# Performance work log

Hardware: AMD Instinct MI355X
Metric: run time of the kernel (lower is better)

Reference implementation:

```python
import jax, jax.numpy as jnp
import numpy as np

EPS = 1e-06


def setup_inputs() -> dict:
    key = jax.random.key(0)
    kq, kk, kv = jax.random.split(key, 3)
    B, H, T, P = 2, 8, 1024, 64
    Q = jax.random.normal(kq, (B, H, T, P), dtype=jnp.float32)
    K = jax.random.normal(kk, (B, H, T, P), dtype=jnp.float32)
    V = jax.random.normal(kv, (B, H, T, P), dtype=jnp.float32)
    return {"Q": Q, "K": K, "V": V}


def _scan_attention(Q, K, V):
    Q_feat = jnp.exp(Q)                                  # (B,H,T,P)
    K_feat = jnp.exp(K)                                  # (B,H,T,P)
    m0 = jnp.log(K_feat)                                 # (B,H,T,P)
    N0 = jnp.einsum('bhtp,bhtn->bhtpn', V, K_feat)       # (B,H,T,P,P) matrix state
    D0 = K_feat                                          # (B,H,T,P)

    def combine(x, y):
        m_x, N_x, D_x = x
        m_y, N_y, D_y = y
        m_new = jnp.maximum(m_x, m_y)
        scale_x = jnp.exp(m_x - m_new)
        scale_y = jnp.exp(m_y - m_new)
        N_new = N_x * scale_x[..., None] + N_y * scale_y[..., None]
        D_new = D_x * scale_x + D_y * scale_y
        return (m_new, N_new, D_new)

    m_cum, num_cum, denom_cum = jax.lax.associative_scan(combine, (m0, N0, D0), axis=2)

    Y_num = jnp.einsum('bhtp,bhtpq->bhtq', Q_feat, num_cum)   # (B,H,T,P)
    Y_den = jnp.einsum('bhtp,bhtp->bht', Q_feat, denom_cum)   # (B,H,T)
    Y = Y_num / (Y_den[..., None] + EPS)
    B, H, T, P = Q.shape
    return Y.transpose(0, 2, 1, 3).reshape(B, T, H * P)


def reference(Q, K, V):
    return _scan_attention(Q, K, V)
```

## Files before the change

### kernel.cpp

```cpp
#include <hip/hip_runtime.h>
#include <hip/hip_bf16.h>

#define TDIM 1024
#define PDIM 64
#define BHN  16
#define NCH  64
#define CHS  16

typedef __bf16 bf16_t;
typedef bf16_t bf16x8 __attribute__((ext_vector_type(8)));
typedef float  floatx4 __attribute__((ext_vector_type(4)));

__device__ __forceinline__ floatx4 mfma16(bf16x8 a, bf16x8 b, floatx4 c) {
    return __builtin_amdgcn_mfma_f32_16x16x32_bf16(a, b, c, 0, 0, 0);
}

__global__ __launch_bounds__(64) void stats_kernel(
        const float* __restrict__ K,
        float* __restrict__ cmax, float* __restrict__ csum) {
    int bh = blockIdx.x >> 6;
    int c  = blockIdx.x & 63;
    int p  = threadIdx.x;
    const float* Kb = K + (size_t)bh * TDIM * PDIM + (size_t)c * CHS * PDIM + p;
    float k[CHS];
#pragma unroll
    for (int i = 0; i < CHS; ++i) k[i] = Kb[i * PDIM];
    float m = -INFINITY, s = 0.f;
#pragma unroll
    for (int i = 0; i < CHS; ++i) {
        m = fmaxf(m, k[i]);
        float e = __expf(k[i]);
        s += e * e;
    }
    cmax[(bh * NCH + c) * PDIM + p] = m;
    csum[(bh * NCH + c) * PDIM + p] = s;
}

__global__ __launch_bounds__(64) void feat_kernel(
        const float* __restrict__ Q, const float* __restrict__ K,
        const float* __restrict__ V,
        const float* __restrict__ cmax, const float* __restrict__ csum,
        bf16_t* __restrict__ W, bf16_t* __restrict__ U,
        bf16_t* __restrict__ Kft, float* __restrict__ den) {
    int bh = blockIdx.x >> 6;
    int c  = blockIdx.x & 63;
    int p  = threadIdx.x;
    size_t base = (size_t)bh * TDIM * PDIM;
    int t0 = c * CHS;

    float m = -INFINITY, s = 0.f;
#pragma unroll 8
    for (int cc = 0; cc < c; ++cc) {
        m = fmaxf(m, cmax[(bh * NCH + cc) * PDIM + p]);
        s += csum[(bh * NCH + cc) * PDIM + p];
    }

    float kq[CHS], qq_[CHS], vv[CHS];
#pragma unroll
    for (int i = 0; i < CHS; ++i) {
        kq[i]  = K[base + (size_t)(t0 + i) * PDIM + p];
        qq_[i] = Q[base + (size_t)(t0 + i) * PDIM + p];
        vv[i]  = V[base + (size_t)(t0 + i) * PDIM + p];
    }

    __shared__ bf16_t ek_t[CHS][PDIM + 4];
    __shared__ float  dt[CHS][PDIM + 1];

#pragma unroll
    for (int i = 0; i < CHS; ++i) {
        int t = t0 + i;
        m = fmaxf(m, kq[i]);
        float ek = __expf(kq[i]);
        s += ek * ek;
        float w = __expf(qq_[i] - m);
        W[base + (size_t)t * PDIM + p] = (bf16_t)w;
        U[base + (size_t)t * PDIM + p] = (bf16_t)(vv[i] * ek);
        ek_t[i][p] = (bf16_t)ek;
        dt[i][p] = w * s;
    }
    __syncthreads();

    {
        int tl = p >> 2, g = p & 3;
        float d = 0.f;
#pragma unroll
        for (int i = 0; i < 16; ++i) d += dt[tl][i * 4 + g];
        d += __shfl_xor(d, 1);
        d += __shfl_xor(d, 2);
        if (g == 0) den[bh * TDIM + t0 + tl] = d;
    }

    {
        int hi = p >> 4, tl = p & 15;
#pragma unroll
        for (int it = 0; it < 16; ++it) {
            int q = it * 4 + hi;
            Kft[((size_t)bh * PDIM + q) * TDIM + t0 + tl] = ek_t[tl][q];
        }
    }
}

__global__ __launch_bounds__(256) void attn_kernel(
        const bf16_t* __restrict__ W, const bf16_t* __restrict__ U,
        const bf16_t* __restrict__ Kft, const float* __restrict__ den,
        float* __restrict__ out) {
    int bh  = blockIdx.x & 15;
    int i   = blockIdx.x >> 4;
    int tid = threadIdx.x;
    int wave = tid >> 6, lane = tid & 63;
    int lq = lane & 15, qd = lane >> 4;
    int b = bh >> 3, h = bh & 7;

    __shared__ bf16_t Wt[64][72];
    __shared__ bf16_t Ut[64][72];
    __shared__ bf16_t Kt[64][72];
    __shared__ bf16_t Ct[64][72];
    __shared__ float  denb[64];

    size_t base = (size_t)bh * TDIM * PDIM;

    {
        const int4* gs = (const int4*)(W + base + (size_t)i * 64 * PDIM);
        for (int r = 0; r < 2; ++r) {
            int idx = tid + r * 256;
            int q = idx >> 3, s = idx & 7;
            *(int4*)&Wt[q][s * 8] = gs[idx];
        }
        if (tid < 64) denb[tid] = den[bh * TDIM + i * 64 + tid];
    }

    floatx4 acc[4];
    for (int j = 0; j < 4; ++j) acc[j] = (floatx4){0.f, 0.f, 0.f, 0.f};

    for (int kt = 0; kt <= i; ++kt) {
        __syncthreads();
        const int4* us = (const int4*)(U + base + (size_t)kt * 64 * PDIM);
        for (int r = 0; r < 2; ++r) {
            int idx = tid + r * 256;
            int q = idx >> 3, s = idx & 7;
            *(int4*)&Ut[q][s * 8] = us[idx];
            const int4* ks2 =
                (const int4*)(Kft + ((size_t)bh * PDIM + q) * TDIM + kt * 64);
            *(int4*)&Kt[q][s * 8] = ks2[s];
        }
        __syncthreads();

        bf16x8 a0 = *(const bf16x8*)&Wt[wave * 16 + lq][qd * 8];
        bf16x8 a1 = *(const bf16x8*)&Wt[wave * 16 + lq][32 + qd * 8];
        floatx4 cc[4];
        for (int j = 0; j < 4; ++j) {
            bf16x8 b0 = *(const bf16x8*)&Ut[j * 16 + lq][qd * 8];
            bf16x8 b1 = *(const bf16x8*)&Ut[j * 16 + lq][32 + qd * 8];
            floatx4 t = (floatx4){0.f, 0.f, 0.f, 0.f};
            t = mfma16(a0, b0, t);
            t = mfma16(a1, b1, t);
            cc[j] = t;
        }

        for (int j = 0; j < 4; ++j) {
            for (int r = 0; r < 4; ++r) {
                int trow = wave * 16 + qd * 4 + r;
                int tcol = j * 16 + lq;
                float v = cc[j][r];
                if (kt == i && tcol > trow) v = 0.f;
                Ct[trow][tcol] = (bf16_t)v;
            }
        }

        for (int ks = 0; ks < 2; ++ks) {
            bf16x8 ca = *(const bf16x8*)&Ct[wave * 16 + lq][ks * 32 + qd * 8];
            for (int j = 0; j < 4; ++j) {
                bf16x8 kb = *(const bf16x8*)&Kt[j * 16 + lq][ks * 32 + qd * 8];
                acc[j] = mfma16(ca, kb, acc[j]);
            }
        }
    }

    for (int j = 0; j < 4; ++j) {
        for (int r = 0; r < 4; ++r) {
            int trow = wave * 16 + qd * 4 + r;
            int tg = i * 64 + trow;
            float y = acc[j][r] / (denb[trow] + 1e-6f);
            out[((size_t)b * TDIM + tg) * (8 * PDIM) + h * PDIM + (j * 16 + lq)] = y;
        }
    }
}

extern "C" void kernel_launch(void* const* d_in, const int* in_sizes, int n_in,
                              void* d_out, int out_size, void* d_ws, size_t ws_size,
                              hipStream_t stream) {
    const float* Q = (const float*)d_in[0];
    const float* K = (const float*)d_in[1];
    const float* V = (const float*)d_in[2];
    float* out = (float*)d_out;

    bf16_t* Wf   = (bf16_t*)d_ws;
    bf16_t* Uf   = Wf + (size_t)BHN * TDIM * PDIM;
    bf16_t* Kft  = Uf + (size_t)BHN * TDIM * PDIM;
    float*  den  = (float*)(Kft + (size_t)BHN * TDIM * PDIM);
    float*  cmax = den + (size_t)BHN * TDIM;
    float*  csum = cmax + (size_t)BHN * NCH * PDIM;

    stats_kernel<<<BHN * NCH, 64, 0, stream>>>(K, cmax, csum);
    feat_kernel<<<BHN * NCH, 64, 0, stream>>>(Q, K, V, cmax, csum, Wf, Uf, Kft, den);
    attn_kernel<<<BHN * 16, 256, 0, stream>>>(Wf, Uf, Kft, den, out);
}
```

Measured before the change: 93.01 us.

## Split attention key tiles across two wave groups and load operands directly to registers

```diff
diff --git a/kernel.cpp b/kernel.cpp
--- a/kernel.cpp
+++ b/kernel.cpp
@@ -100,7 +100,7 @@
     }
 }
 
-__global__ __launch_bounds__(256) void attn_kernel(
+__global__ __launch_bounds__(512, 2) void attn_kernel(
         const bf16_t* __restrict__ W, const bf16_t* __restrict__ U,
         const bf16_t* __restrict__ Kft, const float* __restrict__ den,
         float* __restrict__ out) {
@@ -109,79 +109,92 @@
     int tid = threadIdx.x;
     int wave = tid >> 6, lane = tid & 63;
     int lq = lane & 15, qd = lane >> 4;
+    int sub = wave & 3;
+    int par = wave >> 2;
     int b = bh >> 3, h = bh & 7;
 
-    __shared__ bf16_t Wt[64][72];
-    __shared__ bf16_t Ut[64][72];
-    __shared__ bf16_t Kt[64][72];
-    __shared__ bf16_t Ct[64][72];
+    __shared__ bf16_t Ct[8][16][72];
+    __shared__ float  Yred[4][16][68];
     __shared__ float  denb[64];
 
     size_t base = (size_t)bh * TDIM * PDIM;
-
-    {
-        const int4* gs = (const int4*)(W + base + (size_t)i * 64 * PDIM);
-        for (int r = 0; r < 2; ++r) {
-            int idx = tid + r * 256;
-            int q = idx >> 3, s = idx & 7;
-            *(int4*)&Wt[q][s * 8] = gs[idx];
-        }
-        if (tid < 64) denb[tid] = den[bh * TDIM + i * 64 + tid];
-    }
+    int trow0 = i * 64 + sub * 16;
+
+    if (tid < 64) denb[tid] = den[bh * TDIM + i * 64 + tid];
+
+    const bf16_t* wrow = W + base + (size_t)(trow0 + lq) * PDIM;
+    bf16x8 a0 = *(const bf16x8*)(wrow + qd * 8);
+    bf16x8 a1 = *(const bf16x8*)(wrow + 32 + qd * 8);
 
     floatx4 acc[4];
+#pragma unroll
     for (int j = 0; j < 4; ++j) acc[j] = (floatx4){0.f, 0.f, 0.f, 0.f};
 
-    for (int kt = 0; kt <= i; ++kt) {
-        __syncthreads();
-        const int4* us = (const int4*)(U + base + (size_t)kt * 64 * PDIM);
-        for (int r = 0; r < 2; ++r) {
-            int idx = tid + r * 256;
-            int q = idx >> 3, s = idx & 7;
-            *(int4*)&Ut[q][s * 8] = us[idx];
-            const int4* ks2 =
-                (const int4*)(Kft + ((size_t)bh * PDIM + q) * TDIM + kt * 64);
-            *(int4*)&Kt[q][s * 8] = ks2[s];
-        }
-        __syncthreads();
-
-        bf16x8 a0 = *(const bf16x8*)&Wt[wave * 16 + lq][qd * 8];
-        bf16x8 a1 = *(const bf16x8*)&Wt[wave * 16 + lq][32 + qd * 8];
+    for (int kt = par; kt <= i; kt += 2) {
+        bf16x8 ub[8], kb[8];
+        const bf16_t* ubase = U + base + (size_t)(kt * 64) * PDIM;
+        const bf16_t* kbase = Kft + (size_t)bh * PDIM * TDIM + kt * 64;
+#pragma unroll
+        for (int j = 0; j < 4; ++j) {
+            const bf16_t* ur = ubase + (size_t)(j * 16 + lq) * PDIM;
+            ub[2 * j]     = *(const bf16x8*)(ur + qd * 8);
+            ub[2 * j + 1] = *(const bf16x8*)(ur + 32 + qd * 8);
+        }
+#pragma unroll
+        for (int j = 0; j < 4; ++j) {
+            const bf16_t* kr = kbase + (size_t)(j * 16 + lq) * TDIM;
+            kb[2 * j]     = *(const bf16x8*)(kr + qd * 8);
+            kb[2 * j + 1] = *(const bf16x8*)(kr + 32 + qd * 8);
+        }
+
         floatx4 cc[4];
-        for (int j = 0; j < 4; ++j) {
-            bf16x8 b0 = *(const bf16x8*)&Ut[j * 16 + lq][qd * 8];
-            bf16x8 b1 = *(const bf16x8*)&Ut[j * 16 + lq][32 + qd * 8];
+#pragma unroll
+        for (int j = 0; j < 4; ++j) {
             floatx4 t = (floatx4){0.f, 0.f, 0.f, 0.f};
-            t = mfma16(a0, b0, t);
-            t = mfma16(a1, b1, t);
+            t = mfma16(a0, ub[2 * j], t);
+            t = mfma16(a1, ub[2 * j + 1], t);
             cc[j] = t;
         }
 
-        for (int j = 0; j < 4; ++j) {
+#pragma unroll
+        for (int j = 0; j < 4; ++j) {
+#pragma unroll
             for (int r = 0; r < 4; ++r) {
-                int trow = wave * 16 + qd * 4 + r;
-                int tcol = j * 16 + lq;
                 float v = cc[j][r];
-                if (kt == i && tcol > trow) v = 0.f;
-                Ct[trow][tcol] = (bf16_t)v;
+                if (kt == i && (kt * 64 + j * 16 + lq) > (trow0 + qd * 4 + r))
+                    v = 0.f;
+                Ct[wave][qd * 4 + r][j * 16 + lq] = (bf16_t)v;
             }
         }
 
-        for (int ks = 0; ks < 2; ++ks) {
-            bf16x8 ca = *(const bf16x8*)&Ct[wave * 16 + lq][ks * 32 + qd * 8];
-            for (int j = 0; j < 4; ++j) {
-                bf16x8 kb = *(const bf16x8*)&Kt[j * 16 + lq][ks * 32 + qd * 8];
-                acc[j] = mfma16(ca, kb, acc[j]);
+        bf16x8 ca0 = *(const bf16x8*)&Ct[wave][lq][qd * 8];
+        bf16x8 ca1 = *(const bf16x8*)&Ct[wave][lq][32 + qd * 8];
+#pragma unroll
+        for (int j = 0; j < 4; ++j) {
+            acc[j] = mfma16(ca0, kb[2 * j], acc[j]);
+            acc[j] = mfma16(ca1, kb[2 * j + 1], acc[j]);
+        }
+    }
+
+    if (par == 1) {
+#pragma unroll
+        for (int j = 0; j < 4; ++j)
+#pragma unroll
+            for (int r = 0; r < 4; ++r)
+                Yred[sub][qd * 4 + r][j * 16 + lq] = acc[j][r];
+    }
+    __syncthreads();
+    if (par == 0) {
+#pragma unroll
+        for (int j = 0; j < 4; ++j) {
+#pragma unroll
+            for (int r = 0; r < 4; ++r) {
+                int trow_l = sub * 16 + qd * 4 + r;
+                int tg = i * 64 + trow_l;
+                float y = acc[j][r] + Yred[sub][qd * 4 + r][j * 16 + lq];
+                y = y / (denb[trow_l] + 1e-6f);
+                out[((size_t)b * TDIM + tg) * (8 * PDIM) + h * PDIM + j * 16 + lq] = y;
             }
-        }
-    }
-
-    for (int j = 0; j < 4; ++j) {
-        for (int r = 0; r < 4; ++r) {
-            int trow = wave * 16 + qd * 4 + r;
-            int tg = i * 64 + trow;
-            float y = acc[j][r] / (denb[trow] + 1e-6f);
-            out[((size_t)b * TDIM + tg) * (8 * PDIM) + h * PDIM + (j * 16 + lq)] = y;
         }
     }
 }
@@ -203,5 +216,5 @@
 
     stats_kernel<<<BHN * NCH, 64, 0, stream>>>(K, cmax, csum);
     feat_kernel<<<BHN * NCH, 64, 0, stream>>>(Q, K, V, cmax, csum, Wf, Uf, Kft, den);
-    attn_kernel<<<BHN * 16, 256, 0, stream>>>(Wf, Uf, Kft, den, out);
-}
+    attn_kernel<<<256, 512, 0, stream>>>(Wf, Uf, Kft, den, out);
+}
```

New measurement: 103.7 us. 1.11x slower.
